# Performance work log

Measured on AMD Instinct MI355X. Metric: run time of the kernel, lower is better.

The kernel has to match this reference:

```python
import jax, jax.numpy as jnp
import numpy as np

B, LP, LQ, H = 16, 512, 512, 768


def setup_inputs() -> dict:
    key = jax.random.key(0)
    k0, k1, k2, k3 = jax.random.split(key, 4)
    proj_p = jax.random.normal(k0, (B, LP, H), dtype=jnp.float32)
    proj_q = jax.random.normal(k1, (B, LQ, H), dtype=jnp.float32)
    seq_len = jax.random.randint(k2, (B,), 1, LQ + 1)  # valid lengths in [1, LQ]
    W_trans = jax.random.normal(k3, (H, H), dtype=jnp.float32) / jnp.sqrt(H).astype(jnp.float32)
    b_trans = jnp.zeros((H,), dtype=jnp.float32)
    return {"proj_p": proj_p, "proj_q": proj_q, "seq_len": seq_len,
            "W_trans": W_trans, "b_trans": b_trans}


def reference(proj_p, proj_q, seq_len, W_trans, b_trans):
    # trans_q = trans_linear(proj_q): [B, Lq, H]
    trans_q = jnp.einsum('bqh,oh->bqo', proj_q, W_trans) + b_trans
    # attention scores: [B, Lp, Lq]
    att = jnp.einsum('bph,bqh->bpq', proj_p, trans_q)
    # masked_softmax (MedLane style): softmax(scores * mask), re-mask, renormalize
    mask = (jnp.arange(LQ)[None, None, :] < seq_len[:, None, None]).astype(att.dtype)
    probs = jax.nn.softmax(att * mask, axis=-1) * mask
    probs = probs / (jnp.sum(probs, axis=-1, keepdims=True) + 1e-13)
    # weighted sum of proj_q: [B, Lp, H]
    att_vec = jnp.einsum('bpq,bqh->bph', probs, proj_q)
    # output = ReLU(trans_linear(att_vec))
    out = jax.nn.relu(jnp.einsum('bph,oh->bpo', att_vec, W_trans) + b_trans)
    return out
```

## Files before the change

### kernel.cpp

```cpp
#include <hip/hip_runtime.h>

typedef _Float16 f16x8 __attribute__((ext_vector_type(8)));
typedef __attribute__((ext_vector_type(4))) float f32x4;
typedef unsigned short u16;

__device__ __forceinline__ u16 f2h(float f) {
    _Float16 h = (_Float16)f;
    return __builtin_bit_cast(u16, h);
}

__device__ __forceinline__ f16x8 cvt8(float4 a, float4 b) {
    f16x8 r;
    r[0] = (_Float16)a.x; r[1] = (_Float16)a.y; r[2] = (_Float16)a.z; r[3] = (_Float16)a.w;
    r[4] = (_Float16)b.x; r[5] = (_Float16)b.y; r[6] = (_Float16)b.z; r[7] = (_Float16)b.w;
    return r;
}

#define LGKM0_BAR()                                                            \
    do {                                                                       \
        asm volatile("s_waitcnt lgkmcnt(0)" ::: "memory");                     \
        __builtin_amdgcn_s_barrier();                                          \
    } while (0)

template<bool AF32, bool BF32, int OUT, bool BIAS, bool RELU, bool RS, bool TW,
         int GX, int GY>
__global__ __launch_bounds__(256, 3)
void gemm_nt(const void* __restrict__ Av, const void* __restrict__ Bv,
             const float* __restrict__ bias, const float* __restrict__ rs,
             void* __restrict__ Cv, u16* __restrict__ CT,
             int K, int lda, int ldb, int ldc,
             long sA, long sB, long sC)
{
    __shared__ u16 lds[24576];
    constexpr int BOF  = 8192;
    constexpr int BUFE = 12288;

    const unsigned flat = blockIdx.x;
    const unsigned cpx  = gridDim.x >> 3;
    const unsigned id   = (flat & 7u) * cpx + (flat >> 3);
    const int bz  = (int)(id / (unsigned)(GX * GY));
    const int rem = (int)(id - (unsigned)bz * (GX * GY));
    const int by  = rem / GX;
    const int bx  = rem - by * GX;

    const int tid  = threadIdx.x;
    const int lane = tid & 63;
    const int wid  = tid >> 6;
    const int m0 = by * 128;
    const int n0 = bx * 64;

    const int rowS = tid >> 3;
    const int cg   = tid & 7;
    const int slw  = cg ^ (rowS & 7);

    const float* aF = nullptr; const u16* aH = nullptr;
    const float* bF = nullptr; const u16* bH = nullptr;
    if constexpr (AF32)
        aF = (const float*)Av + (size_t)bz * sA + ((size_t)(m0 + rowS)) * lda + cg * 8;
    else
        aH = (const u16*)Av + (size_t)bz * sA + ((size_t)(m0 + rowS)) * lda + cg * 8;
    if constexpr (BF32)
        bF = (const float*)Bv + (size_t)bz * sB + ((size_t)(n0 + rowS)) * ldb + cg * 8;
    else
        bH = (const u16*)Bv + (size_t)bz * sB + ((size_t)(n0 + rowS)) * ldb + cg * 8;

    const int wm = (wid & 1) * 64;
    const int wn = (wid >> 1) * 32;
    const int fr = lane & 15;
    const int fq = lane >> 4;

    f32x4 acc[4][2] = {};

    float4 rA[8]; f16x8 hA[4];
    float4 rB[4]; f16x8 hB[2];

    auto loadT = [&](int k0) {
        if constexpr (AF32) {
#pragma unroll
            for (int c = 0; c < 4; ++c) {
                const float* p = aF + (size_t)(c * 32) * lda + k0;
                rA[2 * c]     = *(const float4*)p;
                rA[2 * c + 1] = *(const float4*)(p + 4);
            }
        } else {
#pragma unroll
            for (int c = 0; c < 4; ++c)
                hA[c] = *(const f16x8*)(aH + (size_t)(c * 32) * lda + k0);
        }
        if constexpr (BF32) {
#pragma unroll
            for (int c = 0; c < 2; ++c) {
                const float* p = bF + (size_t)(c * 32) * ldb + k0;
                rB[2 * c]     = *(const float4*)p;
                rB[2 * c + 1] = *(const float4*)(p + 4);
            }
        } else {
#pragma unroll
            for (int c = 0; c < 2; ++c)
                hB[c] = *(const f16x8*)(bH + (size_t)(c * 32) * ldb + k0);
        }
    };

    auto writeT = [&](int be) {
#pragma unroll
        for (int c = 0; c < 4; ++c) {
            f16x8 v;
            if constexpr (AF32) v = cvt8(rA[2 * c], rA[2 * c + 1]);
            else                v = hA[c];
            *(f16x8*)(lds + be + (c * 32 + rowS) * 64 + slw * 8) = v;
        }
#pragma unroll
        for (int c = 0; c < 2; ++c) {
            f16x8 v;
            if constexpr (BF32) v = cvt8(rB[2 * c], rB[2 * c + 1]);
            else                v = hB[c];
            *(f16x8*)(lds + be + BOF + (c * 32 + rowS) * 64 + slw * 8) = v;
        }
    };

    auto compute = [&](int be) {
#pragma unroll
        for (int w = 0; w < 2; ++w) {
            const int sw = (((w << 2) | fq) ^ (fr & 7)) << 3;
            f16x8 vah[4], vbh[2];
#pragma unroll
            for (int i = 0; i < 4; ++i)
                vah[i] = *(const f16x8*)(lds + be + (wm + i * 16 + fr) * 64 + sw);
#pragma unroll
            for (int j = 0; j < 2; ++j)
                vbh[j] = *(const f16x8*)(lds + be + BOF + (wn + j * 16 + fr) * 64 + sw);
#pragma unroll
            for (int i = 0; i < 4; ++i)
#pragma unroll
                for (int j = 0; j < 2; ++j)
                    acc[i][j] = __builtin_amdgcn_mfma_f32_16x16x32_f16(vah[i], vbh[j], acc[i][j], 0, 0, 0);
        }
    };

    loadT(0);
    writeT(0);
    loadT(64);
    LGKM0_BAR();
    for (int k0 = 0; k0 < K; k0 += 128) {
        compute(0);
        writeT(BUFE);
        if (k0 + 128 < K) loadT(k0 + 128);
        LGKM0_BAR();
        compute(BUFE);
        if (k0 + 128 < K) {
            writeT(0);
            if (k0 + 192 < K) loadT(k0 + 192);
        }
        LGKM0_BAR();
    }

    float bj[2];
    if (BIAS) {
#pragma unroll
        for (int j = 0; j < 2; ++j) bj[j] = bias[n0 + wn + j * 16 + fr];
    }
    const long crow0 = m0 + wm + fq * 4;
    const long ccol0 = n0 + wn + fr;
    float* Cf = (float*)Cv + (size_t)bz * sC;
    u16*   Ch = (u16*)Cv   + (size_t)bz * sC;
    const float* rsb = RS ? (rs + (size_t)bz * 512) : nullptr;
    const int  bzT = (int)(crow0 >> 9);
    const long qb  = crow0 & 511;
#pragma unroll
    for (int i = 0; i < 4; ++i) {
        float rsv[4];
        if (RS) {
#pragma unroll
            for (int r = 0; r < 4; ++r) rsv[r] = 1.0f - rsb[crow0 + i * 16 + r];
        }
#pragma unroll
        for (int j = 0; j < 2; ++j) {
            ushort4 tw;
#pragma unroll
            for (int r = 0; r < 4; ++r) {
                float v = acc[i][j][r];
                if (BIAS) v += RS ? bj[j] * rsv[r] : bj[j];
                if (RELU) v = fmaxf(v, 0.0f);
                const size_t idx = (size_t)(crow0 + i * 16 + r) * ldc + ccol0 + j * 16;
                if (OUT == 0) Cf[idx] = v;
                else {
                    const u16 h = f2h(v);
                    Ch[idx] = h;
                    if (TW) (&tw.x)[r] = h;
                }
            }
            if (OUT == 1 && TW) {
                *(ushort4*)(CT + (size_t)bzT * 768 * 512
                               + (size_t)(ccol0 + j * 16) * 512 + qb + i * 16) = tw;
            }
        }
    }
}

__global__ __launch_bounds__(256)
void softmax_kernel(float* __restrict__ att, const int* __restrict__ seq_len,
                    float* __restrict__ rsout)
{
    const int row = blockIdx.x;
    const int b   = row >> 9;
    float* s = att + (size_t)row * 512;
    const int L = seq_len[b];
    const int tid = threadIdx.x;

    __shared__ float red[4];

    const float v0 = s[tid];
    const float v1 = s[tid + 256];
    const bool  k0 = (tid < L);
    const bool  k1 = (tid + 256 < L);
    const float s0 = k0 ? v0 : 0.0f;
    const float s1 = k1 ? v1 : 0.0f;

    float m = fmaxf(s0, s1);
#pragma unroll
    for (int o = 32; o > 0; o >>= 1) m = fmaxf(m, __shfl_down(m, o));
    if ((tid & 63) == 0) red[tid >> 6] = m;
    __syncthreads();
    const float M = fmaxf(fmaxf(red[0], red[1]), fmaxf(red[2], red[3]));
    __syncthreads();

    const float e0 = k0 ? expf(s0 - M) : 0.0f;
    const float e1 = k1 ? expf(s1 - M) : 0.0f;

    float zs = e0 + e1;
#pragma unroll
    for (int o = 32; o > 0; o >>= 1) zs += __shfl_down(zs, o);
    if ((tid & 63) == 0) red[tid >> 6] = zs;
    __syncthreads();
    const float sve = red[0] + red[1] + red[2] + red[3];

    const float Z   = sve + (float)(512 - L) * expf(-M);
    const float S   = sve / Z;
    const float inv = 1.0f / (S + 1e-13f);
    const float sc  = inv / Z;

    u16* o16 = (u16*)s;
    o16[tid]       = f2h(k0 ? e0 * sc : 0.0f);
    o16[tid + 256] = f2h(k1 ? e1 * sc : 0.0f);
    if (tid == 0) rsout[row] = S * inv;
}

extern "C" void kernel_launch(void* const* d_in, const int* in_sizes, int n_in,
                              void* d_out, int out_size, void* d_ws, size_t ws_size,
                              hipStream_t stream)
{
    (void)in_sizes; (void)n_in; (void)out_size; (void)ws_size;
    constexpr int B = 16, L = 512, H = 768;
    constexpr size_t NPQ = (size_t)B * L * H;

    const float* proj_p  = (const float*)d_in[0];
    const float* proj_q  = (const float*)d_in[1];
    const int*   seq_len = (const int*)d_in[2];
    const float* W       = (const float*)d_in[3];
    const float* bias    = (const float*)d_in[4];
    float* out = (float*)d_out;

    u16* ws   = (u16*)d_ws;
    u16* tqT  = ws;
    float* att = (float*)(tqT + NPQ);
    float* rs  = att + (size_t)B * L * L;

    u16* tq16 = (u16*)d_out;

    gemm_nt<true, true, 1, true, false, false, true, 12, 64><<<768, 256, 0, stream>>>(
        proj_q, W, bias, nullptr, tq16, tqT, H, H, H, H, 0, 0, 0);

    gemm_nt<true, false, 0, false, false, false, false, 8, 4><<<512, 256, 0, stream>>>(
        proj_p, tq16, nullptr, nullptr, att, nullptr, H, H, H, L,
        (long)L * H, (long)L * H, (long)L * L);

    softmax_kernel<<<B * L, 256, 0, stream>>>(att, seq_len, rs);

    gemm_nt<false, false, 0, true, true, true, false, 12, 4><<<768, 256, 0, stream>>>(
        (const u16*)att, tqT, bias, rs, out, nullptr,
        L, 1024, L, H, (long)L * 1024, (long)H * L, (long)L * H);
}
```

Baseline: 68.30 us.

## Fuse masked softmax into the probability-times-value GEMM

Removes the separate softmax kernel and folds it into the final GEMM. Each block reads its 128 fp32 score rows three times (max, sum, then normalize into fp16 registers), stages the probabilities into LDS as the A operand, and applies the bias-times-(1-rowsum) correction and ReLU in the epilogue. This saves a kernel launch and the fp16 write-back and re-read of the probabilities. In exchange, the fp32 score rows are re-read by every column block (12 per row block), and holding the probability tile in registers raises register pressure.

Result: slower. 157.8 us (+131.0%).

```diff
diff --git a/kernel.cpp b/kernel.cpp
--- a/kernel.cpp
+++ b/kernel.cpp
@@ -22,11 +22,10 @@
         __builtin_amdgcn_s_barrier();                                          \
     } while (0)
 
-template<bool AF32, bool BF32, int OUT, bool BIAS, bool RELU, bool RS, bool TW,
-         int GX, int GY>
+template<bool AF32, bool BF32, int OUT, bool BIAS, bool TW, int GX, int GY>
 __global__ __launch_bounds__(256, 3)
 void gemm_nt(const void* __restrict__ Av, const void* __restrict__ Bv,
-             const float* __restrict__ bias, const float* __restrict__ rs,
+             const float* __restrict__ bias,
              void* __restrict__ Cv, u16* __restrict__ CT,
              int K, int lda, int ldb, int ldc,
              long sA, long sB, long sC)
@@ -163,24 +162,17 @@
     const long ccol0 = n0 + wn + fr;
     float* Cf = (float*)Cv + (size_t)bz * sC;
     u16*   Ch = (u16*)Cv   + (size_t)bz * sC;
-    const float* rsb = RS ? (rs + (size_t)bz * 512) : nullptr;
     const int  bzT = (int)(crow0 >> 9);
     const long qb  = crow0 & 511;
 #pragma unroll
-    for (int i = 0; i < 4; ++i) {
-        float rsv[4];
-        if (RS) {
-#pragma unroll
-            for (int r = 0; r < 4; ++r) rsv[r] = 1.0f - rsb[crow0 + i * 16 + r];
-        }
+    for (int i = 0; i < 4; ++i)
 #pragma unroll
         for (int j = 0; j < 2; ++j) {
             ushort4 tw;
 #pragma unroll
             for (int r = 0; r < 4; ++r) {
                 float v = acc[i][j][r];
-                if (BIAS) v += RS ? bj[j] * rsv[r] : bj[j];
-                if (RELU) v = fmaxf(v, 0.0f);
+                if (BIAS) v += bj[j];
                 const size_t idx = (size_t)(crow0 + i * 16 + r) * ldc + ccol0 + j * 16;
                 if (OUT == 0) Cf[idx] = v;
                 else {
@@ -194,55 +186,182 @@
                                + (size_t)(ccol0 + j * 16) * 512 + qb + i * 16) = tw;
             }
         }
-    }
-}
-
-__global__ __launch_bounds__(256)
-void softmax_kernel(float* __restrict__ att, const int* __restrict__ seq_len,
-                    float* __restrict__ rsout)
+}
+
+template<int GX, int GY>
+__global__ __launch_bounds__(256, 2)
+void gemm_pv_sm(const float* __restrict__ att, const u16* __restrict__ tqT,
+                const float* __restrict__ bias, const int* __restrict__ seq_len,
+                float* __restrict__ out)
 {
-    const int row = blockIdx.x;
-    const int b   = row >> 9;
-    float* s = att + (size_t)row * 512;
-    const int L = seq_len[b];
-    const int tid = threadIdx.x;
-
-    __shared__ float red[4];
-
-    const float v0 = s[tid];
-    const float v1 = s[tid + 256];
-    const bool  k0 = (tid < L);
-    const bool  k1 = (tid + 256 < L);
-    const float s0 = k0 ? v0 : 0.0f;
-    const float s1 = k1 ? v1 : 0.0f;
-
-    float m = fmaxf(s0, s1);
-#pragma unroll
-    for (int o = 32; o > 0; o >>= 1) m = fmaxf(m, __shfl_down(m, o));
-    if ((tid & 63) == 0) red[tid >> 6] = m;
-    __syncthreads();
-    const float M = fmaxf(fmaxf(red[0], red[1]), fmaxf(red[2], red[3]));
-    __syncthreads();
-
-    const float e0 = k0 ? expf(s0 - M) : 0.0f;
-    const float e1 = k1 ? expf(s1 - M) : 0.0f;
-
-    float zs = e0 + e1;
-#pragma unroll
-    for (int o = 32; o > 0; o >>= 1) zs += __shfl_down(zs, o);
-    if ((tid & 63) == 0) red[tid >> 6] = zs;
-    __syncthreads();
-    const float sve = red[0] + red[1] + red[2] + red[3];
-
-    const float Z   = sve + (float)(512 - L) * expf(-M);
-    const float S   = sve / Z;
-    const float inv = 1.0f / (S + 1e-13f);
-    const float sc  = inv / Z;
-
-    u16* o16 = (u16*)s;
-    o16[tid]       = f2h(k0 ? e0 * sc : 0.0f);
-    o16[tid + 256] = f2h(k1 ? e1 * sc : 0.0f);
-    if (tid == 0) rsout[row] = S * inv;
+    __shared__ u16 lds[24576];
+    __shared__ float rs_l[128];
+    constexpr int BOF  = 8192;
+    constexpr int BUFE = 12288;
+
+    const unsigned flat = blockIdx.x;
+    const unsigned cpx  = gridDim.x >> 3;
+    const unsigned id   = (flat & 7u) * cpx + (flat >> 3);
+    const int bz  = (int)(id / (unsigned)(GX * GY));
+    const int rem = (int)(id - (unsigned)bz * (GX * GY));
+    const int by  = rem / GX;
+    const int bx  = rem - by * GX;
+
+    const int tid  = threadIdx.x;
+    const int lane = tid & 63;
+    const int wid  = tid >> 6;
+    const int m0 = by * 128;
+    const int n0 = bx * 64;
+
+    const int rowS = tid >> 3;
+    const int cg   = tid & 7;
+    const int slw  = cg ^ (rowS & 7);
+    const int L    = seq_len[bz];
+
+    const float* aP = att + (size_t)bz * 512 * 512 + (size_t)(m0 + rowS) * 512 + cg * 8;
+    const u16*   bP = tqT + (size_t)bz * 768 * 512 + (size_t)(n0 + rowS) * 512 + cg * 8;
+
+    float mr[4] = {-INFINITY, -INFINITY, -INFINITY, -INFINITY};
+#pragma unroll
+    for (int c = 0; c < 4; ++c)
+#pragma unroll
+        for (int st = 0; st < 8; ++st) {
+            const float* p = aP + (size_t)(c * 32) * 512 + st * 64;
+            float4 a0 = *(const float4*)p;
+            float4 a1 = *(const float4*)(p + 4);
+            const int q0 = st * 64 + cg * 8;
+#pragma unroll
+            for (int e = 0; e < 8; ++e) {
+                const float x = e < 4 ? (&a0.x)[e] : (&a1.x)[e - 4];
+                mr[c] = fmaxf(mr[c], (q0 + e < L) ? x : 0.0f);
+            }
+        }
+#pragma unroll
+    for (int c = 0; c < 4; ++c) {
+        mr[c] = fmaxf(mr[c], __shfl_xor(mr[c], 1));
+        mr[c] = fmaxf(mr[c], __shfl_xor(mr[c], 2));
+        mr[c] = fmaxf(mr[c], __shfl_xor(mr[c], 4));
+    }
+
+    float zr[4] = {};
+#pragma unroll
+    for (int c = 0; c < 4; ++c)
+#pragma unroll
+        for (int st = 0; st < 8; ++st) {
+            const float* p = aP + (size_t)(c * 32) * 512 + st * 64;
+            float4 a0 = *(const float4*)p;
+            float4 a1 = *(const float4*)(p + 4);
+            const int q0 = st * 64 + cg * 8;
+#pragma unroll
+            for (int e = 0; e < 8; ++e) {
+                const float x = e < 4 ? (&a0.x)[e] : (&a1.x)[e - 4];
+                zr[c] += (q0 + e < L) ? __expf(x - mr[c]) : 0.0f;
+            }
+        }
+
+    float sc_c[4];
+#pragma unroll
+    for (int c = 0; c < 4; ++c) {
+        zr[c] += __shfl_xor(zr[c], 1);
+        zr[c] += __shfl_xor(zr[c], 2);
+        zr[c] += __shfl_xor(zr[c], 4);
+        const float Z   = zr[c] + (float)(512 - L) * __expf(-mr[c]);
+        const float S   = zr[c] / Z;
+        const float inv = 1.0f / (S + 1e-13f);
+        sc_c[c] = inv / Z;
+        if (cg == 0) rs_l[c * 32 + rowS] = S * inv;
+    }
+
+    f16x8 P[4][8];
+#pragma unroll
+    for (int c = 0; c < 4; ++c)
+#pragma unroll
+        for (int st = 0; st < 8; ++st) {
+            const float* p = aP + (size_t)(c * 32) * 512 + st * 64;
+            float4 a0 = *(const float4*)p;
+            float4 a1 = *(const float4*)(p + 4);
+            const int q0 = st * 64 + cg * 8;
+            f16x8 ph;
+#pragma unroll
+            for (int e = 0; e < 8; ++e) {
+                const float x = e < 4 ? (&a0.x)[e] : (&a1.x)[e - 4];
+                const float pe = (q0 + e < L) ? __expf(x - mr[c]) * sc_c[c] : 0.0f;
+                ph[e] = (_Float16)pe;
+            }
+            P[c][st] = ph;
+        }
+
+    const int wm = (wid & 1) * 64;
+    const int wn = (wid >> 1) * 32;
+    const int fr = lane & 15;
+    const int fq = lane >> 4;
+
+    f32x4 acc[4][2] = {};
+    f16x8 hB0[2], hB1[2];
+
+    auto loadB = [&](int st, bool set1) {
+        f16x8* h = set1 ? hB1 : hB0;
+#pragma unroll
+        for (int c = 0; c < 2; ++c)
+            h[c] = *(const f16x8*)(bP + (size_t)(c * 32) * 512 + st * 64);
+    };
+    auto writeT = [&](int be, int st, bool set1) {
+        const f16x8* h = set1 ? hB1 : hB0;
+#pragma unroll
+        for (int c = 0; c < 4; ++c)
+            *(f16x8*)(lds + be + (c * 32 + rowS) * 64 + slw * 8) = P[c][st];
+#pragma unroll
+        for (int c = 0; c < 2; ++c)
+            *(f16x8*)(lds + be + BOF + (c * 32 + rowS) * 64 + slw * 8) = h[c];
+    };
+    auto compute = [&](int be) {
+#pragma unroll
+        for (int w = 0; w < 2; ++w) {
+            const int sw = (((w << 2) | fq) ^ (fr & 7)) << 3;
+            f16x8 vah[4], vbh[2];
+#pragma unroll
+            for (int i = 0; i < 4; ++i)
+                vah[i] = *(const f16x8*)(lds + be + (wm + i * 16 + fr) * 64 + sw);
+#pragma unroll
+            for (int j = 0; j < 2; ++j)
+                vbh[j] = *(const f16x8*)(lds + be + BOF + (wn + j * 16 + fr) * 64 + sw);
+#pragma unroll
+            for (int i = 0; i < 4; ++i)
+#pragma unroll
+                for (int j = 0; j < 2; ++j)
+                    acc[i][j] = __builtin_amdgcn_mfma_f32_16x16x32_f16(vah[i], vbh[j], acc[i][j], 0, 0, 0);
+        }
+    };
+
+    loadB(0, false);
+    writeT(0, 0, false);
+    loadB(1, true);
+    LGKM0_BAR();
+#pragma unroll
+    for (int st = 0; st < 8; ++st) {
+        compute((st & 1) ? BUFE : 0);
+        if (st < 7) writeT((st & 1) ? 0 : BUFE, st + 1, !(st & 1));
+        if (st < 6) loadB(st + 2, (st & 1) != 0);
+        LGKM0_BAR();
+    }
+
+    float bj[2];
+#pragma unroll
+    for (int j = 0; j < 2; ++j) bj[j] = bias[n0 + wn + j * 16 + fr];
+    const int  lr0   = wm + fq * 4;
+    const long crow0 = m0 + lr0;
+    const long ccol0 = n0 + wn + fr;
+    float* op = out + (size_t)bz * 512 * 768;
+#pragma unroll
+    for (int i = 0; i < 4; ++i)
+#pragma unroll
+        for (int j = 0; j < 2; ++j)
+#pragma unroll
+            for (int r = 0; r < 4; ++r) {
+                float v = acc[i][j][r] + bj[j] * (1.0f - rs_l[lr0 + i * 16 + r]);
+                v = fmaxf(v, 0.0f);
+                op[(size_t)(crow0 + i * 16 + r) * 768 + ccol0 + j * 16] = v;
+            }
 }
 
 extern "C" void kernel_launch(void* const* d_in, const int* in_sizes, int n_in,
@@ -263,20 +382,15 @@
     u16* ws   = (u16*)d_ws;
     u16* tqT  = ws;
     float* att = (float*)(tqT + NPQ);
-    float* rs  = att + (size_t)B * L * L;
 
     u16* tq16 = (u16*)d_out;
 
-    gemm_nt<true, true, 1, true, false, false, true, 12, 64><<<768, 256, 0, stream>>>(
-        proj_q, W, bias, nullptr, tq16, tqT, H, H, H, H, 0, 0, 0);
-
-    gemm_nt<true, false, 0, false, false, false, false, 8, 4><<<512, 256, 0, stream>>>(
-        proj_p, tq16, nullptr, nullptr, att, nullptr, H, H, H, L,
+    gemm_nt<true, true, 1, true, true, 12, 64><<<768, 256, 0, stream>>>(
+        proj_q, W, bias, tq16, tqT, H, H, H, H, 0, 0, 0);
+
+    gemm_nt<true, false, 0, false, false, 8, 4><<<512, 256, 0, stream>>>(
+        proj_p, tq16, nullptr, att, nullptr, H, H, H, L,
         (long)L * H, (long)L * H, (long)L * L);
 
-    softmax_kernel<<<B * L, 256, 0, stream>>>(att, seq_len, rs);
-
-    gemm_nt<false, false, 0, true, true, true, false, 12, 4><<<768, 256, 0, stream>>>(
-        (const u16*)att, tqT, bias, rs, out, nullptr,
-        L, 1024, L, H, (long)L * 1024, (long)H * L, (long)L * H);
-}
+    gemm_pv_sm<12, 4><<<768, 256, 0, stream>>>(att, tqT, bias, seq_len, out);
+}
```
